# Optimization experiments

Hardware: AMD Instinct MI355X
Metric: run time of the kernel (lower is better)

The kernel has to match this reference:

```python
import jax, jax.numpy as jnp
import numpy as np

T, B, S = 2000, 64, 128   # seq_len, batch, alphabet_len
W = 16                    # beam_width
BLANK = 0                 # blank_index
PRUNE = 0.001             # prune_threshold
NONBLANK = np.array([c for c in range(S) if c != BLANK], dtype=np.int32)  # [S-1]
HASH_MULT = np.uint32(1000003)


def setup_inputs() -> dict:
    key = jax.random.key(0)
    k1, k2 = jax.random.split(key)
    x = jax.random.uniform(k1, (T, B, S), dtype=jnp.float32)
    lengths = jax.random.randint(k2, (B,), T // 2, T + 1, dtype=jnp.int32)
    return {"x": x, "lengths": lengths}


def _decode_one(ctc, length):
    # ctc: [T, S] probabilities for one utterance; length: scalar int32.
    nonblank = jnp.asarray(NONBLANK)
    arW = jnp.arange(W)

    prefixes0 = -jnp.ones((W, T), jnp.int32)          # padded prefixes
    len0 = jnp.zeros((W,), jnp.int32)
    # beam 0 = empty prefix (hash 0); others get unique sentinel hashes, prob 0
    hash0 = jnp.where(arW == 0, jnp.uint32(0),
                      jnp.uint32(0x80000000) + arW.astype(jnp.uint32))
    pb0 = jnp.zeros((W,), jnp.float32).at[0].set(1.0)  # Pb[-1][()] = 1
    pnb0 = jnp.zeros((W,), jnp.float32)                # Pnb[-1][()] = 0

    def step(carry, xs):
        prefixes, plen, h, p_b, p_nb = carry
        probs_raw, t = xs
        # pruning: symbols with prob <= threshold contribute nothing
        probs = jnp.where(probs_raw > PRUNE, probs_raw, 0.0)
        p_tot = p_b + p_nb
        last = jnp.where(plen > 0, prefixes[arW, jnp.maximum(plen - 1, 0)], -1)

        # --- candidates 0..W-1: prefix unchanged ---
        c0_pb = probs[BLANK] * p_tot                              # blank extends
        c0_pnb = jnp.where(last >= 0, probs[last] * p_nb, 0.0)    # repeat-last

        # --- candidates for beam b extended by nonblank symbol c: [W, S-1] ---
        pc = probs[nonblank]                                      # [S-1]
        rep = nonblank[None, :] == last[:, None]                  # [W, S-1]
        e_pnb = pc[None, :] * jnp.where(rep, p_b[:, None], p_tot[:, None])
        e_h = h[:, None] * HASH_MULT + (nonblank.astype(jnp.uint32) + 1)[None, :]
        e_pnb_f = e_pnb.reshape(-1)                               # [W*(S-1)]
        e_h_f = e_h.reshape(-1)

        # Merge: an extension can only coincide with another beam's unchanged
        # prefix (extensions of distinct prefixes are always distinct).
        eq = h[:, None] == e_h_f[None, :]                         # [W, W*(S-1)]
        u_pnb = c0_pnb + eq.astype(jnp.float32) @ e_pnb_f
        u_pb = c0_pb
        dup = eq.any(axis=0)

        key = jnp.concatenate([u_pb + u_pnb, jnp.where(dup, -1.0, e_pnb_f)])
        cand_pb = jnp.concatenate([u_pb, jnp.zeros_like(e_pnb_f)])
        cand_pnb = jnp.concatenate([u_pnb, jnp.where(dup, 0.0, e_pnb_f)])
        cand_h = jnp.concatenate([h, e_h_f])
        _, idx = jax.lax.top_k(key, W)

        ext = idx >= W
        q = jnp.maximum(idx - W, 0)
        nb = jnp.where(ext, q // (S - 1), idx)                    # source beam
        csym = jnp.where(ext, nonblank[q % (S - 1)], -1)          # appended sym
        base_pref = prefixes[nb]
        base_len = plen[nb]
        pos = jnp.arange(T)[None, :]
        n_pref = jnp.where((csym[:, None] >= 0) & (pos == base_len[:, None]),
                           csym[:, None], base_pref)
        n_len = base_len + (csym >= 0).astype(jnp.int32)
        n_h = cand_h[idx]
        n_pb = cand_pb[idx]
        n_pnb = cand_pnb[idx]

        # rescale to avoid fp underflow over long sequences (ranking-preserving;
        # the torch module returns only the argmax prefix, not raw scores)
        scale = 1.0 / jnp.maximum(jnp.max(n_pb + n_pnb), 1e-30)
        n_pb = n_pb * scale
        n_pnb = n_pnb * scale

        valid = t < length
        new = (n_pref, n_len, n_h, n_pb, n_pnb)
        old = (prefixes, plen, h, p_b, p_nb)
        carry = tuple(jnp.where(valid, a, b) for a, b in zip(new, old))
        return carry, None

    carry, _ = jax.lax.scan(jax.checkpoint(step),
                            (prefixes0, len0, hash0, pb0, pnb0),
                            (ctc, jnp.arange(T, dtype=jnp.int32)))
    prefixes, plen, _, p_b, p_nb = carry
    # top_k already sorted beams descending by total prob -> beam 0 is best
    return prefixes[0], plen[0], p_b[0] + p_nb[0]


def reference(x, lengths):
    # x: [T, B, S]; lengths: [B] int32
    prefs, lens, scores = jax.vmap(_decode_one, in_axes=(1, 0))(x, lengths)
    # prefs: [B, T] best prefix per element, padded with -1; lens: [B]
    return prefs, lens, scores
```

## Files before the change

### kernel.cpp

```cpp
#include <hip/hip_runtime.h>
#include <stdint.h>

#define T_ 2000
#define B_ 64
#define S_ 128
#define HASHM 1000003u

typedef float f4 __attribute__((ext_vector_type(4)));
typedef int i2v __attribute__((ext_vector_type(2)));

#if defined(__has_builtin)
#if __has_builtin(__builtin_amdgcn_permlane32_swap)
#define HAVE_PL32 1
#endif
#if __has_builtin(__builtin_amdgcn_permlane16_swap)
#define HAVE_PL16 1
#endif
#endif

__device__ __forceinline__ uint32_t rl(uint32_t v, int ln) {
  return (uint32_t)__builtin_amdgcn_readlane((int)v, ln);
}
__device__ __forceinline__ float rlf(float v, int ln) {
  return __uint_as_float(rl(__float_as_uint(v), ln));
}

__device__ __forceinline__ uint32_t fkey(float v) {
  uint32_t b = __float_as_uint(v);
  return b ^ (((int32_t)b < 0) ? 0xFFFFFFFFu : 0x80000000u);
}

__device__ __forceinline__ void wave_lds_fence() {
  asm volatile("s_waitcnt lgkmcnt(0)" ::: "memory");
}

template<int J>
__device__ __forceinline__ uint32_t bfly_u32(uint32_t v) {
  if constexpr (J == 1)
    return (uint32_t)__builtin_amdgcn_update_dpp((int)v, (int)v, 0xB1, 0xF, 0xF, false);
  else if constexpr (J == 2)
    return (uint32_t)__builtin_amdgcn_update_dpp((int)v, (int)v, 0x4E, 0xF, 0xF, false);
  else if constexpr (J == 4) {
    uint32_t a = (uint32_t)__builtin_amdgcn_update_dpp((int)v, (int)v, 0x12C, 0xF, 0xF, false);
    uint32_t b = (uint32_t)__builtin_amdgcn_update_dpp((int)v, (int)v, 0x124, 0xF, 0xF, false);
    return ((threadIdx.x & 4) == 0) ? a : b;
  } else if constexpr (J == 8)
    return (uint32_t)__builtin_amdgcn_update_dpp((int)v, (int)v, 0x128, 0xF, 0xF, false);
  else if constexpr (J == 16) {
#ifdef HAVE_PL16
    i2v r = __builtin_amdgcn_permlane16_swap((int)v, (int)v, false, false);
    return (uint32_t)(((threadIdx.x & 16) == 0) ? r[1] : r[0]);
#else
    return (uint32_t)__builtin_amdgcn_ds_swizzle((int)v, 0x401F);
#endif
  } else {
#ifdef HAVE_PL32
    i2v r = __builtin_amdgcn_permlane32_swap((int)v, (int)v, false, false);
    return (uint32_t)(((threadIdx.x & 32) == 0) ? r[1] : r[0]);
#else
    return (uint32_t)__shfl_xor((int)v, 32);
#endif
  }
}
template<int J>
__device__ __forceinline__ uint64_t bfly_u64(uint64_t v) {
  uint32_t lo = bfly_u32<J>((uint32_t)v);
  uint32_t hi = bfly_u32<J>((uint32_t)(v >> 32));
  return ((uint64_t)hi << 32) | lo;
}

#define BSTF(KK, J) { float p_ = __uint_as_float(bfly_u32<J>(__float_as_uint(v))); \
  bool d_ = ((ln & (KK)) == 0) == ((ln & (J)) == 0); \
  float mx_ = fmaxf(v, p_), mn_ = fminf(v, p_); v = d_ ? mx_ : mn_; }
#define BST64(KK, J) { uint64_t p_ = bfly_u64<J>(v); \
  bool d_ = ((ln & (KK)) == 0) == ((ln & (J)) == 0); \
  uint64_t mx_ = v > p_ ? v : p_, mn_ = v > p_ ? p_ : v; v = d_ ? mx_ : mn_; }

__device__ __forceinline__ float bsort64_f32(float v, const int ln) {
  BSTF(2, 1)
  BSTF(4, 2) BSTF(4, 1)
  BSTF(8, 4) BSTF(8, 2) BSTF(8, 1)
  BSTF(16, 8) BSTF(16, 4) BSTF(16, 2) BSTF(16, 1)
  BSTF(32, 16) BSTF(32, 8) BSTF(32, 4) BSTF(32, 2) BSTF(32, 1)
  BSTF(64, 32) BSTF(64, 16) BSTF(64, 8) BSTF(64, 4) BSTF(64, 2) BSTF(64, 1)
  return v;
}

template<int WIDTH>
__device__ __forceinline__ uint64_t bsortN_u64(uint64_t v, const int ln) {
  BST64(2, 1)
  BST64(4, 2) BST64(4, 1)
  BST64(8, 4) BST64(8, 2) BST64(8, 1)
  BST64(16, 8) BST64(16, 4) BST64(16, 2) BST64(16, 1)
  if constexpr (WIDTH >= 32) {
    BST64(32, 16) BST64(32, 8) BST64(32, 4) BST64(32, 2) BST64(32, 1)
  }
  if constexpr (WIDTH >= 64) {
    BST64(64, 32) BST64(64, 16) BST64(64, 8) BST64(64, 4) BST64(64, 2) BST64(64, 1)
  }
  return v;
}

__device__ __forceinline__ uint32_t incl_scan_add(uint32_t v) {
  v += (uint32_t)__builtin_amdgcn_update_dpp(0, (int)v, 0x111, 0xF, 0xF, false);
  v += (uint32_t)__builtin_amdgcn_update_dpp(0, (int)v, 0x112, 0xF, 0xF, false);
  v += (uint32_t)__builtin_amdgcn_update_dpp(0, (int)v, 0x114, 0xF, 0xF, false);
  v += (uint32_t)__builtin_amdgcn_update_dpp(0, (int)v, 0x118, 0xF, 0xF, false);
  v += (uint32_t)__builtin_amdgcn_update_dpp(0, (int)v, 0x142, 0xA, 0xF, false);
  v += (uint32_t)__builtin_amdgcn_update_dpp(0, (int)v, 0x143, 0xC, 0xF, false);
  return v;
}

template<int CTRL>
__device__ __forceinline__ uint64_t dpp_max_u64(uint64_t v) {
  uint32_t lo = (uint32_t)v, hi = (uint32_t)(v >> 32);
  uint32_t slo = (uint32_t)__builtin_amdgcn_update_dpp(0, (int)lo, CTRL, 0xF, 0xF, false);
  uint32_t shi = (uint32_t)__builtin_amdgcn_update_dpp(0, (int)hi, CTRL, 0xF, 0xF, false);
  uint64_t o = ((uint64_t)shi << 32) | slo;
  return (o > v) ? o : v;
}
__device__ __forceinline__ uint64_t wave_max_u64(uint64_t v) {
  v = dpp_max_u64<0x111>(v);
  v = dpp_max_u64<0x112>(v);
  v = dpp_max_u64<0x114>(v);
  v = dpp_max_u64<0x118>(v);
  v = dpp_max_u64<0x142>(v);
  v = dpp_max_u64<0x143>(v);
  uint32_t lo = rl((uint32_t)v, 63);
  uint32_t hi = rl((uint32_t)(v >> 32), 63);
  return ((uint64_t)hi << 32) | lo;
}

__global__ __launch_bounds__(64, 1) void ctc_decode_kernel(
    const float* __restrict__ x, const int* __restrict__ lengths,
    float* __restrict__ out) {
  __shared__ uint64_t surv[64];
  __shared__ __align__(16) float Pr[2][S_];
  __shared__ __align__(8) uint16_t trace[T_ * 16];

  const int b = blockIdx.x;
  const int lane = (int)threadIdx.x;
  const int m = lane & 15;
  const int g = lane >> 4;
  const int lenb = lengths[b];

  uint32_t h = (m == 0) ? 0u : (0x80000000u + (uint32_t)m);
  float pb = (m == 0) ? 1.0f : 0.0f;
  float pnb = 0.0f;
  int last = -1;
  int len = 0;

  float cur0;
  {
    const float* xt = x + (size_t)b * S_;
    float a0 = xt[lane], a1 = xt[lane + 64];
    float p0 = (a0 > 0.001f) ? a0 : 0.0f;
    float p1 = (a1 > 0.001f) ? a1 : 0.0f;
    Pr[0][lane] = p0;
    Pr[0][lane + 64] = p1;
    cur0 = p0;
  }

  const uint32_t cbase = 1u + 32u * (uint32_t)g;
  const uint32_t nrefb = ~(15u + (uint32_t)m * 127u + 32u * (uint32_t)g);

  for (int t = 0; t < lenb; ++t) {
    const float* P = Pr[t & 1];
    float r0n = 0.0f, r1n = 0.0f;
    const bool hasNext = (t + 1 < lenb);
    if (hasNext) {
      const float* xt = x + ((size_t)(t + 1) * B_ + b) * S_;
      r0n = xt[lane];
      r1n = xt[lane + 64];
    }
    wave_lds_fence();
    const uint32_t hM = h * HASHM;

    const float ptot = __fadd_rn(pb, pnb);
    const float P0 = rlf(cur0, 0);
    const float c0pb = __fmul_rn(P0, ptot);
    const float plast = P[(last >= 0) ? last : 0];
    const float c0pnb = (last >= 0) ? __fmul_rn(plast, pnb) : 0.0f;

    uint32_t lmask = 0;
    uint32_t dlt[16], ccs[16];
    float tval[16], spb[16], spt[16];
    uint32_t slst[16];
    #pragma unroll
    for (int j = 0; j < 16; ++j) {
      uint32_t s_h = rl(h, j);
      uint32_t p = (s_h - hM) - cbase;
      lmask |= (p < 32u) ? (1u << (p & 31u)) : 0u;
      uint32_t d = h - s_h * HASHM;
      bool match = (d - 2u) <= 126u;
      uint32_t cc = match ? (d - 1u) : 1u;
      dlt[j] = d;
      ccs[j] = cc;
      tval[j] = P[cc];
      spb[j] = rlf(pb, j);
      spt[j] = rlf(ptot, j);
      slst[j] = rl((uint32_t)last, j);
    }
    float term[16];
    #pragma unroll
    for (int j = 0; j < 16; ++j) {
      bool match = (dlt[j] - 2u) <= 126u;
      float sel = (ccs[j] == slst[j]) ? spb[j] : spt[j];
      term[j] = match ? __fmul_rn(tval[j], sel) : 0.0f;
    }
    #pragma unroll
    for (int st = 1; st < 16; st <<= 1) {
      #pragma unroll
      for (int i2 = 0; i2 < 16; i2 += 2 * st)
        term[i2] = __fadd_rn(term[i2], term[i2 + st]);
    }
    const float upnb = __fadd_rn(c0pnb, term[0]);
    const float key16 = __fadd_rn(c0pb, upnb);

    f4 pv[8];
    {
      const f4* P4 = (const f4*)(P + 32 * g);
      #pragma unroll
      for (int i = 0; i < 8; ++i) pv[i] = P4[i];
    }
    const int lk = last - 32 * g;
    float kf[32];
    #pragma unroll
    for (int k = 0; k < 32; ++k) {
      float pc = pv[k >> 2][k & 3];
      float sel = (k == lk) ? pb : ptot;
      float val = __fmul_rn(pc, sel);
      bool dup = (lmask >> k) & 1u;
      float kv = dup ? -1.0f : val;
      if (k == 0) kv = (lane < 16) ? key16 : kv;
      kf[k] = kv;
    }

    float t1[16], t2[16];
    #pragma unroll
    for (int i = 0; i < 16; ++i) {
      float a2 = kf[2 * i], b2 = kf[2 * i + 1];
      t1[i] = fmaxf(a2, b2);
      t2[i] = fminf(a2, b2);
    }
    #pragma unroll
    for (int w2 = 8; w2 >= 1; w2 >>= 1) {
      #pragma unroll
      for (int i = 0; i < w2; ++i) {
        float A = t1[i], Bv = t1[i + w2];
        float sa = t2[i], sb = t2[i + w2];
        t1[i] = fmaxf(A, Bv);
        t2[i] = fmaxf(fminf(A, Bv), fmaxf(sa, sb));
      }
    }
    const float m1 = t1[0], m2 = t2[0];

    float th = rlf(bsort64_f32(m1, lane), 15);

    uint32_t gcnt[4];
    #pragma unroll
    for (int grp = 0; grp < 4; ++grp) {
      uint32_t c2 = 0;
      #pragma unroll
      for (int k = grp * 8; k < grp * 8 + 8; ++k) c2 += (kf[k] >= th) ? 1u : 0u;
      gcnt[grp] = c2;
    }
    uint32_t cnt = (gcnt[0] + gcnt[1]) + (gcnt[2] + gcnt[3]);
    uint32_t incl = incl_scan_add(cnt);
    uint32_t M = rl(incl, 63);

    if (__builtin_expect(M > 64u, 0)) {
      float th2 = rlf(bsort64_f32(m2, lane), 7);
      th = fmaxf(th, th2);
      #pragma unroll
      for (int grp = 0; grp < 4; ++grp) {
        uint32_t c2 = 0;
        #pragma unroll
        for (int k = grp * 8; k < grp * 8 + 8; ++k) c2 += (kf[k] >= th) ? 1u : 0u;
        gcnt[grp] = c2;
      }
      cnt = (gcnt[0] + gcnt[1]) + (gcnt[2] + gcnt[3]);
      incl = incl_scan_add(cnt);
      M = rl(incl, 63);
    }

    uint64_t selpk;
    if (__builtin_expect(M <= 64u, 1)) {
      uint64_t* dump = (uint64_t*)(&trace[(size_t)t * 16]);
      uint32_t base0 = incl - cnt;
      uint32_t base1 = base0 + gcnt[0];
      uint32_t base2 = base1 + gcnt[1];
      uint32_t base3 = base2 + gcnt[2];
      uint32_t bases[4] = {base0, base1, base2, base3};
      #pragma unroll
      for (int grp = 0; grp < 4; ++grp) {
        uint32_t pos = bases[grp];
        #pragma unroll
        for (int kk = 0; kk < 8; ++kk) {
          int k = grp * 8 + kk;
          bool q = kf[k] >= th;
          uint32_t nr = nrefb - (uint32_t)k;
          if (k == 0) nr = (lane < 16) ? ~(uint32_t)m : nr;
          uint64_t pk = ((uint64_t)__float_as_uint(kf[k]) << 32) | nr;
          uint64_t* dst = q ? &surv[pos] : dump;
          *dst = pk;
          pos += q ? 1u : 0u;
        }
      }
      wave_lds_fence();
      uint64_t w = ((uint32_t)lane < M) ? surv[lane] : 0ull;
      if (M <= 16u)      w = bsortN_u64<16>(w, lane);
      else if (M <= 32u) w = bsortN_u64<32>(w, lane);
      else               w = bsortN_u64<64>(w, lane);
      uint64_t s16 = bfly_u64<16>(w);
      uint64_t w01 = ((lane & 16) == 0) ? w : s16;
      uint64_t s32 = bfly_u64<32>(w01);
      selpk = ((lane & 32) == 0) ? w01 : s32;
    } else {
      uint32_t alive = 0xFFFFFFFFu;
      selpk = 0;
      #pragma unroll 1
      for (int r = 0; r < 16; ++r) {
        float bk = -1.0f;
        uint32_t bi = 0;
        #pragma unroll
        for (int k = 0; k < 32; ++k) {
          float kv = ((alive >> k) & 1u) ? kf[k] : -1.0f;
          if (kv > bk) { bk = kv; bi = (uint32_t)k; }
        }
        uint32_t nr = nrefb - bi;
        nr = (bi == 0u && lane < 16) ? ~(uint32_t)m : nr;
        uint64_t cand = ((uint64_t)fkey(bk) << 32) | nr;
        uint64_t win = wave_max_u64(cand);
        if (cand == win) alive &= ~(1u << bi);
        if (r == m) selpk = win;
      }
      uint32_t kb = (uint32_t)(selpk >> 32);
      kb ^= ((int32_t)kb < 0) ? 0x80000000u : 0xFFFFFFFFu;
      selpk = ((uint64_t)kb << 32) | (uint32_t)selpk;
    }

    if (hasNext) {
      float p0 = (r0n > 0.001f) ? r0n : 0.0f;
      float p1 = (r1n > 0.001f) ? r1n : 0.0f;
      float* Pn = Pr[(t + 1) & 1];
      Pn[lane] = p0;
      Pn[lane + 64] = p1;
      cur0 = p0;
    }

    const uint32_t gref = ~((uint32_t)selpk);
    const uint32_t keyw = (uint32_t)(selpk >> 32);
    const bool unch = gref < 16u;
    const uint32_t qq = gref - 16u;
    const uint32_t bsrc = qq / 127u;
    const uint32_t jj = qq - bsrc * 127u;
    const uint32_t c = jj + 1u;
    const int srcl = unch ? (int)gref : (int)bsrc;

    const uint32_t s_h = (uint32_t)__shfl((int)h, srcl);
    const uint32_t lpack = ((uint32_t)(last + 1) & 0xFFu) | ((uint32_t)len << 8);
    const uint32_t s_lp = (uint32_t)__shfl((int)lpack, srcl);
    const float s_upb = __shfl(c0pb, srcl);
    const float s_upn = __shfl(upnb, srcl);
    const int s_lst = (int)(s_lp & 0xFFu) - 1;
    const int s_len = (int)(s_lp >> 8);

    const uint32_t n_h = unch ? s_h : (s_h * HASHM + (jj + 2u));
    const float n_pb = unch ? s_upb : 0.0f;
    const float n_pnb = unch ? s_upn : __uint_as_float(keyw);
    const int n_last = unch ? s_lst : (int)c;
    const int n_len = unch ? s_len : (s_len + 1);

    if (lane < 16) {
      trace[t * 16 + lane] =
          (uint16_t)(((uint32_t)srcl << 8) | (unch ? 0u : c));
    }

    const float mxf = fmaxf(__uint_as_float(rl(keyw, 0)), 1e-30f);
    const float scale = __fdiv_rn(1.0f, mxf);
    pb = __fmul_rn(n_pb, scale);
    pnb = __fmul_rn(n_pnb, scale);
    h = n_h; last = n_last; len = n_len;
  }

  __syncthreads();

  float* prefs = out;
  float* lensOut = out + (B_ * T_);
  float* scores = out + (B_ * T_) + B_;

  const int L0 = __shfl(len, 0);
  for (int i = L0 + lane; i < T_; i += 64) prefs[(size_t)b * T_ + i] = -1.0f;

  if (lane == 0) {
    lensOut[b] = (float)L0;
    scores[b] = __fadd_rn(pb, pnb);
    int w = 0;
    int pos2 = L0 - 1;
    for (int t2 = lenb - 1; t2 >= 0; --t2) {
      uint32_t rec = trace[t2 * 16 + w];
      uint32_t sym = rec & 0xFFu;
      if (sym) { prefs[(size_t)b * T_ + pos2] = (float)sym; --pos2; }
      w = (int)(rec >> 8);
    }
  }
}

extern "C" void kernel_launch(void* const* d_in, const int* in_sizes, int n_in,
                              void* d_out, int out_size, void* d_ws, size_t ws_size,
                              hipStream_t stream) {
  (void)in_sizes; (void)n_in; (void)d_ws; (void)ws_size; (void)out_size;
  const float* x = (const float*)d_in[0];
  const int* lengths = (const int*)d_in[1];
  float* out = (float*)d_out;
  ctc_decode_kernel<<<B_, 64, 0, stream>>>(x, lengths, out);
}
```

Measured before the change: 7.903 ms.

## Predict top-k threshold from previous step and fast-path single prefix merge

The kernel now reuses the previous step's 16th-best score, rescaled and halved, as a speculative threshold for the candidate count. It falls back to the full max/second-max reduction and 64-lane bitonic sort only when the surviving count falls outside 16..64. The prefix-merge term is also computed with a single shuffle-based lookup when no beam has more than one matching parent, avoiding 16 readlanes and a reduction tree. The cost is extra branches and a possible double count when the prediction misses.

```diff
diff --git a/kernel.cpp b/kernel.cpp
--- a/kernel.cpp
+++ b/kernel.cpp
@@ -149,6 +149,7 @@
   float pnb = 0.0f;
   int last = -1;
   int len = 0;
+  float thn = 1e30f;
 
   float cur0;
   {
@@ -175,6 +176,7 @@
     }
     wave_lds_fence();
     const uint32_t hM = h * HASHM;
+    const uint32_t hMc = hM + cbase;
 
     const float ptot = __fadd_rn(pb, pnb);
     const float P0 = rlf(cur0, 0);
@@ -183,38 +185,49 @@
     const float c0pnb = (last >= 0) ? __fmul_rn(plast, pnb) : 0.0f;
 
     uint32_t lmask = 0;
-    uint32_t dlt[16], ccs[16];
-    float tval[16], spb[16], spt[16];
-    uint32_t slst[16];
+    uint32_t matchcnt = 0, jm = 0, cc = 1;
     #pragma unroll
     for (int j = 0; j < 16; ++j) {
       uint32_t s_h = rl(h, j);
-      uint32_t p = (s_h - hM) - cbase;
+      uint32_t p = s_h - hMc;
       lmask |= (p < 32u) ? (1u << (p & 31u)) : 0u;
       uint32_t d = h - s_h * HASHM;
       bool match = (d - 2u) <= 126u;
-      uint32_t cc = match ? (d - 1u) : 1u;
-      dlt[j] = d;
-      ccs[j] = cc;
-      tval[j] = P[cc];
-      spb[j] = rlf(pb, j);
-      spt[j] = rlf(ptot, j);
-      slst[j] = rl((uint32_t)last, j);
-    }
-    float term[16];
-    #pragma unroll
-    for (int j = 0; j < 16; ++j) {
-      bool match = (dlt[j] - 2u) <= 126u;
-      float sel = (ccs[j] == slst[j]) ? spb[j] : spt[j];
-      term[j] = match ? __fmul_rn(tval[j], sel) : 0.0f;
-    }
-    #pragma unroll
-    for (int st = 1; st < 16; st <<= 1) {
-      #pragma unroll
-      for (int i2 = 0; i2 < 16; i2 += 2 * st)
-        term[i2] = __fadd_rn(term[i2], term[i2 + st]);
-    }
-    const float upnb = __fadd_rn(c0pnb, term[0]);
+      cc = match ? (d - 1u) : cc;
+      jm = match ? (uint32_t)j : jm;
+      matchcnt += match ? 1u : 0u;
+    }
+
+    float term0;
+    if (__builtin_expect(__ballot(matchcnt > 1u) == 0ull, 1)) {
+      float tpb = __shfl(pb, (int)jm);
+      float tpt = __shfl(ptot, (int)jm);
+      int tlast = __shfl(last, (int)jm);
+      float tv = P[cc];
+      float sel = ((int)cc == tlast) ? tpb : tpt;
+      term0 = (matchcnt != 0u) ? __fmul_rn(tv, sel) : 0.0f;
+    } else {
+      float term[16];
+      #pragma unroll
+      for (int j = 0; j < 16; ++j) {
+        uint32_t s_h = rl(h, j);
+        uint32_t d = h - s_h * HASHM;
+        bool match2 = (d - 2u) <= 126u;
+        uint32_t cc2 = match2 ? (d - 1u) : 1u;
+        float tv = P[cc2];
+        uint32_t slst = rl((uint32_t)last, j);
+        float sel = (cc2 == slst) ? rlf(pb, j) : rlf(ptot, j);
+        term[j] = match2 ? __fmul_rn(tv, sel) : 0.0f;
+      }
+      #pragma unroll
+      for (int st = 1; st < 16; st <<= 1) {
+        #pragma unroll
+        for (int i2 = 0; i2 < 16; i2 += 2 * st)
+          term[i2] = __fadd_rn(term[i2], term[i2 + st]);
+      }
+      term0 = term[0];
+    }
+    const float upnb = __fadd_rn(c0pnb, term0);
     const float key16 = __fadd_rn(c0pb, upnb);
 
     f4 pv[8];
@@ -236,55 +249,57 @@
       kf[k] = kv;
     }
 
-    float t1[16], t2[16];
-    #pragma unroll
-    for (int i = 0; i < 16; ++i) {
-      float a2 = kf[2 * i], b2 = kf[2 * i + 1];
-      t1[i] = fmaxf(a2, b2);
-      t2[i] = fminf(a2, b2);
-    }
-    #pragma unroll
-    for (int w2 = 8; w2 >= 1; w2 >>= 1) {
-      #pragma unroll
-      for (int i = 0; i < w2; ++i) {
-        float A = t1[i], Bv = t1[i + w2];
-        float sa = t2[i], sb = t2[i + w2];
-        t1[i] = fmaxf(A, Bv);
-        t2[i] = fmaxf(fminf(A, Bv), fmaxf(sa, sb));
-      }
-    }
-    const float m1 = t1[0], m2 = t2[0];
-
-    float th = rlf(bsort64_f32(m1, lane), 15);
-
-    uint32_t gcnt[4];
-    #pragma unroll
-    for (int grp = 0; grp < 4; ++grp) {
-      uint32_t c2 = 0;
-      #pragma unroll
-      for (int k = grp * 8; k < grp * 8 + 8; ++k) c2 += (kf[k] >= th) ? 1u : 0u;
-      gcnt[grp] = c2;
-    }
-    uint32_t cnt = (gcnt[0] + gcnt[1]) + (gcnt[2] + gcnt[3]);
-    uint32_t incl = incl_scan_add(cnt);
-    uint32_t M = rl(incl, 63);
-
-    if (__builtin_expect(M > 64u, 0)) {
-      float th2 = rlf(bsort64_f32(m2, lane), 7);
-      th = fmaxf(th, th2);
+    uint32_t gcnt[4], cnt = 0, incl = 0, M = 0;
+    auto do_count = [&](float thv) {
       #pragma unroll
       for (int grp = 0; grp < 4; ++grp) {
         uint32_t c2 = 0;
         #pragma unroll
-        for (int k = grp * 8; k < grp * 8 + 8; ++k) c2 += (kf[k] >= th) ? 1u : 0u;
+        for (int k = grp * 8; k < grp * 8 + 8; ++k)
+          c2 += (kf[k] >= thv) ? 1u : 0u;
         gcnt[grp] = c2;
       }
       cnt = (gcnt[0] + gcnt[1]) + (gcnt[2] + gcnt[3]);
       incl = incl_scan_add(cnt);
       M = rl(incl, 63);
+    };
+
+    float th = thn;
+    do_count(th);
+    if (__builtin_expect(M > 64u, 0)) {
+      th = __fmul_rn(th, 2.0f);
+      do_count(th);
+    }
+    if (__builtin_expect(M < 16u || M > 64u, 0)) {
+      float t1[16], t2[16];
+      #pragma unroll
+      for (int i = 0; i < 16; ++i) {
+        float a2 = kf[2 * i], b2 = kf[2 * i + 1];
+        t1[i] = fmaxf(a2, b2);
+        t2[i] = fminf(a2, b2);
+      }
+      #pragma unroll
+      for (int w2 = 8; w2 >= 1; w2 >>= 1) {
+        #pragma unroll
+        for (int i = 0; i < w2; ++i) {
+          float A = t1[i], Bv = t1[i + w2];
+          float sa = t2[i], sb = t2[i + w2];
+          t1[i] = fmaxf(A, Bv);
+          t2[i] = fmaxf(fminf(A, Bv), fmaxf(sa, sb));
+        }
+      }
+      const float m1 = t1[0], m2 = t2[0];
+      th = rlf(bsort64_f32(m1, lane), 15);
+      do_count(th);
+      if (__builtin_expect(M > 64u, 0)) {
+        float th2 = rlf(bsort64_f32(m2, lane), 7);
+        th = fmaxf(th, th2);
+        do_count(th);
+      }
     }
 
     uint64_t selpk;
+    uint32_t k15raw;
     if (__builtin_expect(M <= 64u, 1)) {
       uint64_t* dump = (uint64_t*)(&trace[(size_t)t * 16]);
       uint32_t base0 = incl - cnt;
@@ -312,12 +327,14 @@
       if (M <= 16u)      w = bsortN_u64<16>(w, lane);
       else if (M <= 32u) w = bsortN_u64<32>(w, lane);
       else               w = bsortN_u64<64>(w, lane);
+      k15raw = rl((uint32_t)(w >> 32), 15);
       uint64_t s16 = bfly_u64<16>(w);
       uint64_t w01 = ((lane & 16) == 0) ? w : s16;
       uint64_t s32 = bfly_u64<32>(w01);
       selpk = ((lane & 32) == 0) ? w01 : s32;
     } else {
       uint32_t alive = 0xFFFFFFFFu;
+      uint32_t k15fk = 0;
       selpk = 0;
       #pragma unroll 1
       for (int r = 0; r < 16; ++r) {
@@ -334,10 +351,12 @@
         uint64_t win = wave_max_u64(cand);
         if (cand == win) alive &= ~(1u << bi);
         if (r == m) selpk = win;
+        if (r == 15) k15fk = (uint32_t)(win >> 32);
       }
       uint32_t kb = (uint32_t)(selpk >> 32);
       kb ^= ((int32_t)kb < 0) ? 0x80000000u : 0xFFFFFFFFu;
       selpk = ((uint64_t)kb << 32) | (uint32_t)selpk;
+      k15raw = k15fk ^ (((int32_t)k15fk < 0) ? 0x80000000u : 0xFFFFFFFFu);
     }
 
     if (hasNext) {
@@ -382,6 +401,9 @@
     pb = __fmul_rn(n_pb, scale);
     pnb = __fmul_rn(n_pnb, scale);
     h = n_h; last = n_last; len = n_len;
+
+    const float k15f = __uint_as_float(k15raw);
+    thn = (k15f > 0.0f) ? __fmul_rn(__fmul_rn(k15f, scale), 0.5f) : 1e30f;
   }
 
   __syncthreads();
```

New measurement: 8.401 ms. 6.3% more time.
